# Kernel optimization log

Measured on AMD Instinct MI355X. Metric: run time of the kernel, lower is better.

## Reference

```python
import jax, jax.numpy as jnp
import numpy as np
from jax import lax

B, P, K = 16, 1024, 32          # clouds, points per cloud, kNN neighbors
N = B * P
NCLS = 40
DIMS = [3, 64, 128, 256]


def setup_inputs() -> dict:
    key = jax.random.key(0)
    ks = jax.random.split(key, 16)
    inp = {
        "x": jax.random.normal(ks[0], (N, DIMS[0]), dtype=jnp.float32),
        "batch": jnp.repeat(jnp.arange(B, dtype=jnp.int64), P),
        "target": jax.random.randint(ks[1], (N,), 0, NCLS, dtype=jnp.int64),
    }
    for i, (fi, fo) in enumerate(zip(DIMS[:-1], DIMS[1:])):
        scale = 1.0 / np.sqrt(2 * fi)
        inp[f"W{i+1}"] = jax.random.normal(ks[2 + 2 * i], (2 * fi, fo), dtype=jnp.float32) * scale
        inp[f"b{i+1}"] = jnp.zeros((fo,), dtype=jnp.float32)
    inp["Wc"] = jax.random.normal(ks[10], (DIMS[-1], NCLS), dtype=jnp.float32) * (1.0 / np.sqrt(DIMS[-1]))
    inp["bc"] = jnp.zeros((NCLS,), dtype=jnp.float32)
    return inp


def knn_graph(x):
    """Per-cloud kNN (loop=False). x: [N,F] with nodes grouped in B clouds of P.
    Returns global neighbor indices [N, K]."""
    xb = x.reshape(B, P, -1)
    sq = jnp.sum(xb * xb, axis=-1)                       # [B,P]
    d2 = sq[:, :, None] + sq[:, None, :] - 2.0 * jnp.einsum("bpf,bqf->bpq", xb, xb)
    d2 = d2 + jnp.eye(P, dtype=x.dtype) * jnp.finfo(x.dtype).max  # exclude self-loops
    _, idx = lax.top_k(-d2, K)                           # [B,P,K] local indices
    gidx = idx + (jnp.arange(B) * P)[:, None, None]      # local -> global node ids
    return gidx.reshape(N, K)


def edge_conv(x, nbr, W, b):
    """EdgeConv: max_j MLP([x_i, x_j - x_i])."""
    xj = x[nbr]                                          # [N,K,F] gather
    xi = x[:, None, :]
    feat = jnp.concatenate([jnp.broadcast_to(xi, xj.shape), xj - xi], axis=-1)  # [N,K,2F]
    h = jnp.einsum("nkf,fo->nko", feat, W) + b           # [N,K,F']
    return jnp.max(h, axis=1)                            # max aggregation


def reference(x, batch, target, W1, b1, W2, b2, W3, b3, Wc, bc):
    del batch  # structure encoded as B clouds of P contiguous nodes
    for W, b in ((W1, b1), (W2, b2), (W3, b3)):
        nbr = knn_graph(x)                               # dynamic graph per layer
        x = jax.nn.relu(edge_conv(x, nbr, W, b))
    logits = x @ Wc + bc                                 # [N, NCLS]
    probs = jax.nn.softmax(logits, axis=-1)
    logp = jax.nn.log_softmax(logits, axis=-1)           # == probs.log()
    loss = -jnp.mean(jnp.take_along_axis(logp, target[:, None], axis=-1))
    return loss, probs
```

## Files before the change

kernel.cpp:

```cpp
#include <hip/hip_runtime.h>
#include <float.h>
#include <math.h>

#define BCLOUDS 16
#define PPTS    1024
#define NPTS    (BCLOUDS * PPTS)
#define KNB     32
#define NCLS    40
#define RPB     4
#define KNNBLK  (NPTS / RPB)
#define EDGEBLK (NPTS / 16)
#define NBIN    256
#define HPADW   (NBIN + NBIN / 16)
#define SELFM   0xFFFFFFFFu

__device__ __forceinline__ int hidx(int b) { return b + (b >> 4); }

template<int F>
__global__ __launch_bounds__(256) void xpose_kernel(const float* __restrict__ x,
                                                    float* __restrict__ xT,
                                                    float* __restrict__ qn) {
    const int p = blockIdx.x * 256 + threadIdx.x;
    const int cloud = p >> 10, pl = p & 1023;
    const float* xr = x + (size_t)p * F;
    float* xTc = xT + (size_t)cloud * F * PPTS;
    float s = 0.f;
    for (int f = 0; f < F; ++f) {
        const float v = xr[f];
        s = fmaf(v, v, s);
        xTc[(size_t)f * PPTS + pl] = v;
    }
    qn[p] = s;
}

template<int F, int FO>
__global__ __launch_bounds__(256, 2) void knn_edge_kernel(const float* __restrict__ x,
                                                          const float* __restrict__ xT,
                                                          const float* __restrict__ qn,
                                                          int* __restrict__ nbr,
                                                          const float* __restrict__ W,
                                                          const float* __restrict__ bias,
                                                          float* __restrict__ A,
                                                          float* __restrict__ Bm) {
    __shared__ unsigned dmat[RPB][PPTS];
    __shared__ float    xp[RPB][F];
    __shared__ float    rn[RPB];
    __shared__ unsigned hist[RPB][HPADW];
    __shared__ float    xs[16][F];

    const int tid = threadIdx.x;

    if (blockIdx.x >= KNNBLK) {
        constexpr int RT  = 16;
        constexpr int RS  = 256 / FO;
        constexpr int RPT = RT / RS;
        const int n0 = (int)(blockIdx.x - KNNBLK) * RT;
        for (int i = tid; i < RT * F; i += 256)
            xs[i / F][i % F] = x[(size_t)n0 * F + i];
        __syncthreads();

        const int o  = tid % FO;
        const int r0 = tid / FO;
        float accA[RPT], accB[RPT];
#pragma unroll
        for (int i = 0; i < RPT; ++i) { accA[i] = 0.f; accB[i] = 0.f; }

        for (int f = 0; f < F; ++f) {
            const float wt = W[(size_t)f * FO + o];
            const float wb = W[(size_t)(F + f) * FO + o];
            const float wd = wt - wb;
#pragma unroll
            for (int i = 0; i < RPT; ++i) {
                const float xv = xs[r0 + i * RS][f];
                accA[i] = fmaf(xv, wd, accA[i]);
                accB[i] = fmaf(xv, wb, accB[i]);
            }
        }
        const float bo = bias[o];
#pragma unroll
        for (int i = 0; i < RPT; ++i) {
            const size_t row = (size_t)(n0 + r0 + i * RS);
            A[row * FO + o]  = accA[i] + bo;
            Bm[row * FO + o] = accB[i];
        }
        return;
    }

    const int lane  = tid & 63;
    const int wave  = tid >> 6;
    const int bid   = blockIdx.x;
    const int cloud = (bid & 7) + 8 * (bid >> 11);
    const int pl0   = ((bid >> 3) & 255) * RPB;

    const float* xc = x + (size_t)cloud * PPTS * F;
    for (int i = tid; i < RPB * F; i += 256)
        xp[i / F][i % F] = xc[(size_t)(pl0 + i / F) * F + (i % F)];
    __syncthreads();
    if (tid < RPB) {
        float s = 0.f;
        for (int f = 0; f < F; ++f) { const float v = xp[tid][f]; s = fmaf(v, v, s); }
        rn[tid] = s;
    }
    __syncthreads();

    const float* xTc = xT + (size_t)cloud * F * PPTS;
    const float4 qv = *reinterpret_cast<const float4*>(&qn[cloud * PPTS + 4 * tid]);

    float acc[RPB][4];
#pragma unroll
    for (int r = 0; r < RPB; ++r)
#pragma unroll
        for (int c = 0; c < 4; ++c) acc[r][c] = 0.f;

    if constexpr (F % 4 == 0) {
#pragma unroll 2
        for (int f4 = 0; f4 < F / 4; ++f4) {
            float4 vf[4];
#pragma unroll
            for (int j = 0; j < 4; ++j)
                vf[j] = *reinterpret_cast<const float4*>(&xTc[(size_t)(4 * f4 + j) * PPTS + 4 * tid]);
            float4 xr[RPB];
#pragma unroll
            for (int r = 0; r < RPB; ++r) xr[r] = *reinterpret_cast<const float4*>(&xp[r][4 * f4]);
#pragma unroll
            for (int r = 0; r < RPB; ++r) {
                acc[r][0] = fmaf(vf[0].x, xr[r].x, acc[r][0]);
                acc[r][1] = fmaf(vf[0].y, xr[r].x, acc[r][1]);
                acc[r][2] = fmaf(vf[0].z, xr[r].x, acc[r][2]);
                acc[r][3] = fmaf(vf[0].w, xr[r].x, acc[r][3]);
                acc[r][0] = fmaf(vf[1].x, xr[r].y, acc[r][0]);
                acc[r][1] = fmaf(vf[1].y, xr[r].y, acc[r][1]);
                acc[r][2] = fmaf(vf[1].z, xr[r].y, acc[r][2]);
                acc[r][3] = fmaf(vf[1].w, xr[r].y, acc[r][3]);
                acc[r][0] = fmaf(vf[2].x, xr[r].z, acc[r][0]);
                acc[r][1] = fmaf(vf[2].y, xr[r].z, acc[r][1]);
                acc[r][2] = fmaf(vf[2].z, xr[r].z, acc[r][2]);
                acc[r][3] = fmaf(vf[2].w, xr[r].z, acc[r][3]);
                acc[r][0] = fmaf(vf[3].x, xr[r].w, acc[r][0]);
                acc[r][1] = fmaf(vf[3].y, xr[r].w, acc[r][1]);
                acc[r][2] = fmaf(vf[3].z, xr[r].w, acc[r][2]);
                acc[r][3] = fmaf(vf[3].w, xr[r].w, acc[r][3]);
            }
        }
    } else {
        for (int f = 0; f < F; ++f) {
            const float4 v = *reinterpret_cast<const float4*>(&xTc[(size_t)f * PPTS + 4 * tid]);
#pragma unroll
            for (int r = 0; r < RPB; ++r) {
                const float xv = xp[r][f];
                acc[r][0] = fmaf(v.x, xv, acc[r][0]);
                acc[r][1] = fmaf(v.y, xv, acc[r][1]);
                acc[r][2] = fmaf(v.z, xv, acc[r][2]);
                acc[r][3] = fmaf(v.w, xv, acc[r][3]);
            }
        }
    }
#pragma unroll
    for (int r = 0; r < RPB; ++r) {
        uint4 wv;
        float d2;
        d2 = fmaxf(rn[r] + qv.x - 2.f * acc[r][0], 0.f);
        wv.x = (4 * tid + 0 == pl0 + r) ? SELFM : __float_as_uint(d2);
        d2 = fmaxf(rn[r] + qv.y - 2.f * acc[r][1], 0.f);
        wv.y = (4 * tid + 1 == pl0 + r) ? SELFM : __float_as_uint(d2);
        d2 = fmaxf(rn[r] + qv.z - 2.f * acc[r][2], 0.f);
        wv.z = (4 * tid + 2 == pl0 + r) ? SELFM : __float_as_uint(d2);
        d2 = fmaxf(rn[r] + qv.w - 2.f * acc[r][3], 0.f);
        wv.w = (4 * tid + 3 == pl0 + r) ? SELFM : __float_as_uint(d2);
        *reinterpret_cast<uint4*>(&dmat[r][4 * tid]) = wv;
    }
    __syncthreads();

    unsigned* hw = hist[wave];
    const int r = wave;
    unsigned bits[16];
#pragma unroll
    for (int i = 0; i < 16; ++i) bits[i] = dmat[r][lane + i * 64];

    unsigned m = bits[0];
#pragma unroll
    for (int i = 1; i < 16; ++i) m = min(m, bits[i]);
    unsigned gmin = m;
    unsigned tmax = (lane < 32) ? m : 0u;
#pragma unroll
    for (int off = 1; off < 64; off <<= 1) {
        gmin = min(gmin, (unsigned)__shfl_xor((int)gmin, off));
        tmax = max(tmax, (unsigned)__shfl_xor((int)tmax, off));
    }

    unsigned sm = 0u, nam = 0xFFFFu;
    int R = KNB;
    unsigned base = gmin;
    int shift = 0;
    bool do_hist = tmax > gmin;
    if (do_hist) {
        const unsigned span = tmax - gmin;
        const int lg = 31 - __clz(span);
        shift = lg > 7 ? lg - 7 : 0;
    }

#pragma unroll 1
    for (int pass = 0; pass < 2 && do_hist; ++pass) {
        int bin[16];
#pragma unroll
        for (int j = 0; j < 5; ++j) { const int k2 = lane + j * 64; if (k2 < HPADW) hw[k2] = 0u; }
#pragma unroll
        for (int i = 0; i < 16; ++i) {
            if ((nam >> i) & 1) {
                const unsigned d = bits[i] - base;
                int b = (int)(d >> shift);
                b = b > 255 ? 255 : b;
                bin[i] = b;
                atomicAdd(&hw[hidx(b)], 1u);
            } else bin[i] = 256;
        }
        unsigned h[4];
        int cnt = 0;
#pragma unroll
        for (int j = 0; j < 4; ++j) { h[j] = hw[hidx(lane * 4 + j)]; cnt += (int)h[j]; }
        int inc = cnt;
#pragma unroll
        for (int off = 1; off < 64; off <<= 1) {
            const int nv = __shfl_up(inc, off);
            if (lane >= off) inc += nv;
        }
        const int pre = inc - cnt;
        const bool found = (pre < R && R <= inc);
        unsigned pk = 0;
        if (found) {
            int c = pre, bb = -1, cb = 0; unsigned hbv = 0;
#pragma unroll
            for (int j = 0; j < 4; ++j) {
                if (bb < 0) {
                    if (c + (int)h[j] >= R) { bb = lane * 4 + j; hbv = h[j]; cb = c; }
                    else c += (int)h[j];
                }
            }
            pk = (unsigned)bb | ((unsigned)cb << 8) | (hbv << 16);
        }
        const unsigned long long fm = __ballot(found);
        pk = (unsigned)__shfl((int)pk, __ffsll(fm) - 1);
        const int bbin = (int)(pk & 255u);
        const int cb   = (int)((pk >> 8) & 255u);
        const int hb   = (int)(pk >> 16);
        const int need = R - cb;
        unsigned nnam = 0u;
#pragma unroll
        for (int i = 0; i < 16; ++i) {
            if (bin[i] < bbin) sm |= 1u << i;
            else if (bin[i] == bbin) nnam |= 1u << i;
        }
        if (hb == need && bbin != 255) {
            sm |= nnam; R = 0; do_hist = false;
        } else {
            nam = nnam; R = need;
            if (R <= 4 || shift == 0) do_hist = false;
            else {
                base += (unsigned)bbin << shift;
                shift = shift > 8 ? shift - 8 : 0;
            }
        }
    }

#pragma unroll 1
    while (R > 0) {
        unsigned lmin = 0xFFFFFFFFu;
#pragma unroll
        for (int i = 0; i < 16; ++i)
            if ((nam >> i) & 1) lmin = min(lmin, bits[i]);
        unsigned vmin = lmin;
#pragma unroll
        for (int off = 1; off < 64; off <<= 1)
            vmin = min(vmin, (unsigned)__shfl_xor((int)vmin, off));
        unsigned eq = 0u;
#pragma unroll
        for (int i = 0; i < 16; ++i)
            if (((nam >> i) & 1) && bits[i] == vmin) eq |= 1u << i;
        int tot = __popc(eq);
#pragma unroll
        for (int off = 1; off < 64; off <<= 1) tot += __shfl_xor(tot, off);
        if (tot <= R) { sm |= eq; nam &= ~eq; R -= tot; }
        else {
#pragma unroll
            for (int i = 0; i < 16; ++i) {
                if (R > 0) {
                    const bool c2 = (eq >> i) & 1;
                    const unsigned long long mb = __ballot(c2);
                    const int t2 = (int)__popcll(mb);
                    if (t2 <= R) { if (c2) sm |= 1u << i; R -= t2; }
                    else {
                        const unsigned long long lower = mb & ((1ull << lane) - 1ull);
                        if (c2 && (int)__popcll(lower) < R) sm |= 1u << i;
                        R = 0;
                    }
                }
            }
        }
    }

    int* out = nbr + (size_t)(cloud * PPTS + pl0 + r) * KNB;
    int tot = 0;
#pragma unroll
    for (int i = 0; i < 16; ++i) {
        const bool c2 = (sm >> i) & 1;
        const unsigned long long mb = __ballot(c2);
        if (c2) {
            const int slot = tot + (int)__popcll(mb & ((1ull << lane) - 1ull));
            if (slot < KNB) out[slot] = cloud * PPTS + lane + i * 64;
        }
        tot += (int)__popcll(mb);
    }
    if (lane == 0)
        for (int s = tot; s < KNB; ++s) out[s] = cloud * PPTS + pl0 + r;
}

template<int FO>
__global__ __launch_bounds__(256) void combine_kernel(const float* __restrict__ A,
                                                      const float* __restrict__ Bm,
                                                      const int* __restrict__ nbr,
                                                      float* __restrict__ xout) {
    constexpr int FO4 = FO / 4;
    const int bid = (int)((blockIdx.x & 7) * (gridDim.x >> 3) + (blockIdx.x >> 3));
    const int idx = bid * 256 + threadIdx.x;
    const int n  = idx / FO4;
    const int o4 = idx % FO4;
    const int* nb = nbr + (size_t)n * KNB;
    const float4* B4 = reinterpret_cast<const float4*>(Bm);
    float4 mx = make_float4(-FLT_MAX, -FLT_MAX, -FLT_MAX, -FLT_MAX);
#pragma unroll 8
    for (int k = 0; k < KNB; ++k) {
        const float4 v = B4[(size_t)nb[k] * FO4 + o4];
        mx.x = fmaxf(mx.x, v.x); mx.y = fmaxf(mx.y, v.y);
        mx.z = fmaxf(mx.z, v.z); mx.w = fmaxf(mx.w, v.w);
    }
    const float4 a = reinterpret_cast<const float4*>(A)[idx];
    float4 rr;
    rr.x = fmaxf(a.x + mx.x, 0.f);
    rr.y = fmaxf(a.y + mx.y, 0.f);
    rr.z = fmaxf(a.z + mx.z, 0.f);
    rr.w = fmaxf(a.w + mx.w, 0.f);
    reinterpret_cast<float4*>(xout)[idx] = rr;
}

__global__ __launch_bounds__(320) void cls_gemm_kernel(const float* __restrict__ x,
                                                       const float* __restrict__ Wc,
                                                       const float* __restrict__ bc,
                                                       float* __restrict__ logits) {
    constexpr int RT = 16;
    __shared__ float xs[RT][256];
    __shared__ float wsm[256][NCLS];
    const int tid = threadIdx.x;
    const int n0  = blockIdx.x * RT;

    const float4* xsrc = reinterpret_cast<const float4*>(x + (size_t)n0 * 256);
    float4* xdst = reinterpret_cast<float4*>(&xs[0][0]);
    for (int i = tid; i < RT * 256 / 4; i += 320) xdst[i] = xsrc[i];
    for (int i = tid; i < 256 * NCLS; i += 320) wsm[i / NCLS][i % NCLS] = Wc[i];
    __syncthreads();

    const int o  = tid % NCLS;
    const int rg = tid / NCLS;
    float acc0 = 0.f, acc1 = 0.f;
#pragma unroll 4
    for (int f4 = 0; f4 < 64; ++f4) {
        float wv0 = wsm[4 * f4 + 0][o];
        float wv1 = wsm[4 * f4 + 1][o];
        float wv2 = wsm[4 * f4 + 2][o];
        float wv3 = wsm[4 * f4 + 3][o];
        const float4 xa = *reinterpret_cast<const float4*>(&xs[rg][4 * f4]);
        const float4 xb = *reinterpret_cast<const float4*>(&xs[rg + 8][4 * f4]);
        acc0 = fmaf(xa.x, wv0, acc0); acc0 = fmaf(xa.y, wv1, acc0);
        acc0 = fmaf(xa.z, wv2, acc0); acc0 = fmaf(xa.w, wv3, acc0);
        acc1 = fmaf(xb.x, wv0, acc1); acc1 = fmaf(xb.y, wv1, acc1);
        acc1 = fmaf(xb.z, wv2, acc1); acc1 = fmaf(xb.w, wv3, acc1);
    }
    const float bo = bc[o];
    logits[(size_t)(n0 + rg) * NCLS + o]     = acc0 + bo;
    logits[(size_t)(n0 + rg + 8) * NCLS + o] = acc1 + bo;
}

__global__ __launch_bounds__(256) void softmax_loss_kernel(const float* __restrict__ logits,
                                                           const int* __restrict__ target,
                                                           float* __restrict__ probs,
                                                           float* __restrict__ lossbuf) {
    const int tid = threadIdx.x;
    const int lane = tid & 63;
    const int n = blockIdx.x * 4 + (tid >> 6);
    float logit = -FLT_MAX;
    if (lane < NCLS) logit = logits[(size_t)n * NCLS + lane];
    float m = logit;
#pragma unroll
    for (int off = 32; off; off >>= 1) m = fmaxf(m, __shfl_xor(m, off));
    const float e = (lane < NCLS) ? __expf(logit - m) : 0.f;
    float s = e;
#pragma unroll
    for (int off = 32; off; off >>= 1) s += __shfl_xor(s, off);
    if (lane < NCLS) probs[(size_t)n * NCLS + lane] = e / s;
    const float lt = __shfl(logit, target[n]);
    if (lane == 0) lossbuf[n] = logf(s) - (lt - m);
}

__global__ __launch_bounds__(256) void loss_reduce_kernel(const float* __restrict__ lossbuf,
                                                          float* __restrict__ out) {
    __shared__ float s[256];
    float acc = 0.f;
    for (int i = threadIdx.x; i < NPTS; i += 256) acc += lossbuf[i];
    s[threadIdx.x] = acc;
    __syncthreads();
    for (int off = 128; off; off >>= 1) {
        if (threadIdx.x < off) s[threadIdx.x] += s[threadIdx.x + off];
        __syncthreads();
    }
    if (threadIdx.x == 0) out[0] = s[0] / (float)NPTS;
}

extern "C" void kernel_launch(void* const* d_in, const int* in_sizes, int n_in,
                              void* d_out, int out_size, void* d_ws, size_t ws_size,
                              hipStream_t stream) {
    (void)in_sizes; (void)n_in; (void)out_size; (void)ws_size;
    const float* x_in   = (const float*)d_in[0];
    const int*   target = (const int*)d_in[2];
    const float* W1 = (const float*)d_in[3];
    const float* b1 = (const float*)d_in[4];
    const float* W2 = (const float*)d_in[5];
    const float* b2 = (const float*)d_in[6];
    const float* W3 = (const float*)d_in[7];
    const float* b3 = (const float*)d_in[8];
    const float* Wc = (const float*)d_in[9];
    const float* bc = (const float*)d_in[10];

    char* ws = (char*)d_ws;
    float* X       = (float*)(ws);
    float* xT      = (float*)(ws + (size_t)8  * 1024 * 1024);
    float* A       = (float*)(ws + (size_t)16 * 1024 * 1024);
    float* Bm      = (float*)(ws + (size_t)32 * 1024 * 1024);
    int*   nbr     = (int*)  (ws + (size_t)48 * 1024 * 1024);
    float* lossbuf = (float*)(ws + (size_t)50 * 1024 * 1024);
    float* qn      = lossbuf;
    float* logits  = (float*)(ws + (size_t)16 * 1024 * 1024);

    float* outF  = (float*)d_out;
    float* probs = outF + 1;

    xpose_kernel<3><<<NPTS / 256, 256, 0, stream>>>(x_in, xT, qn);
    knn_edge_kernel<3, 64><<<KNNBLK + EDGEBLK, 256, 0, stream>>>(x_in, xT, qn, nbr, W1, b1, A, Bm);
    combine_kernel<64><<<NPTS * 16 / 256, 256, 0, stream>>>(A, Bm, nbr, X);

    xpose_kernel<64><<<NPTS / 256, 256, 0, stream>>>(X, xT, qn);
    knn_edge_kernel<64, 128><<<KNNBLK + EDGEBLK, 256, 0, stream>>>(X, xT, qn, nbr, W2, b2, A, Bm);
    combine_kernel<128><<<NPTS * 32 / 256, 256, 0, stream>>>(A, Bm, nbr, X);

    xpose_kernel<128><<<NPTS / 256, 256, 0, stream>>>(X, xT, qn);
    knn_edge_kernel<128, 256><<<KNNBLK + EDGEBLK, 256, 0, stream>>>(X, xT, qn, nbr, W3, b3, A, Bm);
    combine_kernel<256><<<NPTS * 64 / 256, 256, 0, stream>>>(A, Bm, nbr, X);

    cls_gemm_kernel<<<NPTS / 16, 320, 0, stream>>>(X, Wc, bc, logits);
    softmax_loss_kernel<<<NPTS / 4, 256, 0, stream>>>(logits, target, probs, lossbuf);
    loss_reduce_kernel<<<1, 256, 0, stream>>>(lossbuf, outF);
}
```

Baseline: 345.2 us.

## Pack kNN histogram bins into 16-bit halves and use ballot-based prefix scan

The per-row radix-select in the kNN kernel now reads distances with vectorized uint4 LDS loads, which changes the point-to-lane mapping. Histogram bins are packed two per 32-bit word, halving the histogram memory and its clearing. The shuffle-based prefix scan is replaced with a bit-sliced ballot/popcount scan, and shfl is replaced with readlane. The self-point is masked out up front, and tie breaking now picks the lowest index one at a time. These changes aim to cut LDS traffic and shuffle latency in the selection phase, but they alter tie-break order and add an iterative loop on ties.

```diff
diff --git a/kernel.cpp b/kernel.cpp
--- a/kernel.cpp
+++ b/kernel.cpp
@@ -10,11 +10,11 @@
 #define RPB     4
 #define KNNBLK  (NPTS / RPB)
 #define EDGEBLK (NPTS / 16)
-#define NBIN    256
-#define HPADW   (NBIN + NBIN / 16)
+#define HWORDS  128
+#define WPADW   (HWORDS + HWORDS / 16)
 #define SELFM   0xFFFFFFFFu
 
-__device__ __forceinline__ int hidx(int b) { return b + (b >> 4); }
+__device__ __forceinline__ int widx(int w) { return w + (w >> 4); }
 
 template<int F>
 __global__ __launch_bounds__(256) void xpose_kernel(const float* __restrict__ x,
@@ -45,7 +45,7 @@
     __shared__ unsigned dmat[RPB][PPTS];
     __shared__ float    xp[RPB][F];
     __shared__ float    rn[RPB];
-    __shared__ unsigned hist[RPB][HPADW];
+    __shared__ unsigned histw[RPB][WPADW];
     __shared__ float    xs[16][F];
 
     const int tid = threadIdx.x;
@@ -171,11 +171,16 @@
     }
     __syncthreads();
 
-    unsigned* hw = hist[wave];
+    unsigned* hw = histw[wave];
     const int r = wave;
+    const unsigned long long lmask = (1ull << lane) - 1ull;
     unsigned bits[16];
 #pragma unroll
-    for (int i = 0; i < 16; ++i) bits[i] = dmat[r][lane + i * 64];
+    for (int c = 0; c < 4; ++c) {
+        const uint4 bv = *reinterpret_cast<const uint4*>(&dmat[r][4 * lane + 256 * c]);
+        bits[4 * c + 0] = bv.x; bits[4 * c + 1] = bv.y;
+        bits[4 * c + 2] = bv.z; bits[4 * c + 3] = bv.w;
+    }
 
     unsigned m = bits[0];
 #pragma unroll
@@ -188,7 +193,11 @@
         tmax = max(tmax, (unsigned)__shfl_xor((int)tmax, off));
     }
 
-    unsigned sm = 0u, nam = 0xFFFFu;
+    unsigned am = 0u;
+#pragma unroll
+    for (int i = 0; i < 16; ++i) am |= (bits[i] <= tmax) ? (1u << i) : 0u;
+
+    unsigned sm = 0u, nam = am;
     int R = KNB;
     unsigned base = gmin;
     int shift = 0;
@@ -203,28 +212,29 @@
     for (int pass = 0; pass < 2 && do_hist; ++pass) {
         int bin[16];
 #pragma unroll
-        for (int j = 0; j < 5; ++j) { const int k2 = lane + j * 64; if (k2 < HPADW) hw[k2] = 0u; }
+        for (int j = 0; j < 3; ++j) { const int k2 = lane + j * 64; if (k2 < WPADW) hw[k2] = 0u; }
 #pragma unroll
         for (int i = 0; i < 16; ++i) {
             if ((nam >> i) & 1) {
-                const unsigned d = bits[i] - base;
-                int b = (int)(d >> shift);
+                int b = (int)((bits[i] - base) >> shift);
                 b = b > 255 ? 255 : b;
                 bin[i] = b;
-                atomicAdd(&hw[hidx(b)], 1u);
+                atomicAdd(&hw[widx(b >> 1)], 1u << ((b & 1) << 4));
             } else bin[i] = 256;
         }
+        const unsigned w0 = hw[widx(2 * lane)];
+        const unsigned w1 = hw[widx(2 * lane + 1)];
         unsigned h[4];
-        int cnt = 0;
-#pragma unroll
-        for (int j = 0; j < 4; ++j) { h[j] = hw[hidx(lane * 4 + j)]; cnt += (int)h[j]; }
-        int inc = cnt;
-#pragma unroll
-        for (int off = 1; off < 64; off <<= 1) {
-            const int nv = __shfl_up(inc, off);
-            if (lane >= off) inc += nv;
-        }
-        const int pre = inc - cnt;
+        h[0] = w0 & 0xFFFFu; h[1] = w0 >> 16;
+        h[2] = w1 & 0xFFFFu; h[3] = w1 >> 16;
+        const int cnt = (int)(h[0] + h[1] + h[2] + h[3]);
+        int pre = 0;
+#pragma unroll
+        for (int b = 0; b < 11; ++b) {
+            const unsigned long long mk = __ballot((cnt >> b) & 1);
+            pre += (int)__popcll(mk & lmask) << b;
+        }
+        const int inc = pre + cnt;
         const bool found = (pre < R && R <= inc);
         unsigned pk = 0;
         if (found) {
@@ -239,7 +249,8 @@
             pk = (unsigned)bb | ((unsigned)cb << 8) | (hbv << 16);
         }
         const unsigned long long fm = __ballot(found);
-        pk = (unsigned)__shfl((int)pk, __ffsll(fm) - 1);
+        const int srcl = (int)__ffsll(fm) - 1;
+        pk = (unsigned)__builtin_amdgcn_readlane((int)pk, srcl);
         const int bbin = (int)(pk & 255u);
         const int cb   = (int)((pk >> 8) & 255u);
         const int hb   = (int)(pk >> 16);
@@ -250,7 +261,7 @@
             if (bin[i] < bbin) sm |= 1u << i;
             else if (bin[i] == bbin) nnam |= 1u << i;
         }
-        if (hb == need && bbin != 255) {
+        if (hb == need) {
             sm |= nnam; R = 0; do_hist = false;
         } else {
             nam = nnam; R = need;
@@ -279,21 +290,23 @@
         int tot = __popc(eq);
 #pragma unroll
         for (int off = 1; off < 64; off <<= 1) tot += __shfl_xor(tot, off);
-        if (tot <= R) { sm |= eq; nam &= ~eq; R -= tot; }
-        else {
-#pragma unroll
-            for (int i = 0; i < 16; ++i) {
-                if (R > 0) {
-                    const bool c2 = (eq >> i) & 1;
-                    const unsigned long long mb = __ballot(c2);
-                    const int t2 = (int)__popcll(mb);
-                    if (t2 <= R) { if (c2) sm |= 1u << i; R -= t2; }
-                    else {
-                        const unsigned long long lower = mb & ((1ull << lane) - 1ull);
-                        if (c2 && (int)__popcll(lower) < R) sm |= 1u << i;
-                        R = 0;
+        if (tot <= R) {
+            sm |= eq; nam &= ~eq; R -= tot;
+        } else {
+#pragma unroll 1
+            while (R > 0) {
+                int mq = 4096, ms = -1;
+#pragma unroll
+                for (int i = 0; i < 16; ++i)
+                    if ((eq >> i) & 1) {
+                        const int qi = 4 * lane + (i & 3) + 256 * (i >> 2);
+                        if (qi < mq) { mq = qi; ms = i; }
                     }
-                }
+                int gq = mq;
+#pragma unroll
+                for (int off = 1; off < 64; off <<= 1) gq = min(gq, __shfl_xor(gq, off));
+                if (mq == gq && ms >= 0) { sm |= 1u << ms; eq &= ~(1u << ms); }
+                --R;
             }
         }
     }
@@ -305,8 +318,8 @@
         const bool c2 = (sm >> i) & 1;
         const unsigned long long mb = __ballot(c2);
         if (c2) {
-            const int slot = tot + (int)__popcll(mb & ((1ull << lane) - 1ull));
-            if (slot < KNB) out[slot] = cloud * PPTS + lane + i * 64;
+            const int slot = tot + (int)__popcll(mb & lmask);
+            if (slot < KNB) out[slot] = cloud * PPTS + 4 * lane + (i & 3) + 256 * (i >> 2);
         }
         tot += (int)__popcll(mb);
     }
```

Measured after the change: 333.0 us. 3.5% less time.
